# Kernel optimization log

Measured on AMD Instinct MI355X. Metric: run time of the kernel, lower is better.

## Reference

```python
import jax, jax.numpy as jnp
import numpy as np

B, S = 256, 32
XSIZE, YSIZE = 64, 64
LABEL_SIZE = 24
DEFAULT_LABEL = 0


def setup_inputs() -> dict:
    key = jax.random.key(0)
    ks = jax.random.split(key, 12)
    inp = {
        'pred_left': jax.random.normal(ks[0], (B, S, XSIZE), jnp.float32),
        'pred_top': jax.random.normal(ks[1], (B, S, YSIZE), jnp.float32),
        'pred_width': jax.random.normal(ks[2], (B, S, XSIZE), jnp.float32),
        'pred_height': jax.random.normal(ks[3], (B, S, YSIZE), jnp.float32),
        'pred_label': jax.random.normal(ks[4], (B, S, LABEL_SIZE), jnp.float32),
        'true_left': jax.random.randint(ks[5], (B, S), 0, XSIZE, jnp.int32),
        'true_top': jax.random.randint(ks[6], (B, S), 0, YSIZE, jnp.int32),
        'true_width': jax.random.randint(ks[7], (B, S), 0, 32, jnp.int32),
        'true_height': jax.random.randint(ks[8], (B, S), 0, 32, jnp.int32),
        'true_label': jax.random.randint(ks[9], (B, S), 0, LABEL_SIZE, jnp.int32),
        'true_length': jax.random.randint(ks[10], (B,), 0, S + 1, jnp.int32),
        'pred_length': jax.random.randint(ks[11], (B,), 0, S + 1, jnp.int32),
    }
    return inp


def _make_gridmaps(left, top, width, height, label, mask):
    right = jnp.minimum(XSIZE - 1, left + width)    # [B,S]
    bottom = jnp.minimum(YSIZE - 1, top + height)   # [B,S]
    # original skips boxes with top>=bottom or left>=right
    valid = mask & (top < bottom) & (left < right)
    ys = jnp.arange(YSIZE, dtype=jnp.int32)
    xs = jnp.arange(XSIZE, dtype=jnp.int32)
    cov_y = (top[:, :, None] <= ys) & (ys <= bottom[:, :, None])   # [B,S,Y]
    cov_x = (left[:, :, None] <= xs) & (xs <= right[:, :, None])   # [B,S,X]
    cover = valid[:, :, None, None] & cov_y[:, :, :, None] & cov_x[:, :, None, :]  # [B,S,Y,X]
    j = jnp.arange(S, dtype=jnp.int32)
    last = jnp.max(jnp.where(cover, j[None, :, None, None], -1), axis=1)  # [B,Y,X]
    gathered = jnp.take_along_axis(
        label, jnp.clip(last, 0, S - 1).reshape(label.shape[0], -1), axis=1
    ).reshape(last.shape)
    return jnp.where(last >= 0, gathered, DEFAULT_LABEL)


def _compute_acc_miou(map_true, map_pred):
    b = map_true.shape[0]
    bidx = jnp.arange(b, dtype=jnp.int32)[:, None]
    pred = map_pred.reshape(b, -1)
    true = map_true.reshape(b, -1)
    confusion = jnp.zeros((b, LABEL_SIZE, LABEL_SIZE), jnp.int32).at[bidx, pred, true].add(1)
    confusion = confusion.astype(jnp.float32)
    inter = jnp.diagonal(confusion, axis1=1, axis2=2)
    union = confusion.sum(axis=1) + confusion.sum(axis=2) - inter
    acc = inter.sum(axis=1) / confusion.sum(axis=(1, 2))
    weight = (union > 0).astype(jnp.float32)
    iou = inter / (union + 1e-9)
    miou = (weight * iou).sum(axis=1) / weight.sum(axis=1)
    return acc, miou


def reference(pred_left, pred_top, pred_width, pred_height, pred_label,
              true_left, true_top, true_width, true_height, true_label,
              true_length, pred_length):
    seq = jnp.arange(S, dtype=jnp.int32)
    mask_true = seq[None, :] < true_length[:, None]
    mask_pred = seq[None, :] < pred_length[:, None]
    map_true = _make_gridmaps(true_left, true_top, true_width, true_height,
                              true_label, mask_true)
    # from_logits: argmax over last dim (stop_gradient in original)
    pl = jnp.argmax(jax.lax.stop_gradient(pred_left), axis=-1).astype(jnp.int32)
    pt = jnp.argmax(jax.lax.stop_gradient(pred_top), axis=-1).astype(jnp.int32)
    pw = jnp.argmax(jax.lax.stop_gradient(pred_width), axis=-1).astype(jnp.int32)
    ph = jnp.argmax(jax.lax.stop_gradient(pred_height), axis=-1).astype(jnp.int32)
    plab = jnp.argmax(jax.lax.stop_gradient(pred_label), axis=-1).astype(jnp.int32)
    map_pred = _make_gridmaps(pl, pt, pw, ph, plab, mask_pred)
    acc, miou = _compute_acc_miou(map_true, map_pred)
    return acc, miou
```

## Files before the change

kernel.cpp:

```cpp
#include <hip/hip_runtime.h>

#define NB 256
#define S  32
#define NL 24

__global__ __launch_bounds__(256) void layout_metric_kernel(
    const float* __restrict__ pred_left,
    const float* __restrict__ pred_top,
    const float* __restrict__ pred_width,
    const float* __restrict__ pred_height,
    const float* __restrict__ pred_label,
    const int* __restrict__ true_left,
    const int* __restrict__ true_top,
    const int* __restrict__ true_width,
    const int* __restrict__ true_height,
    const int* __restrict__ true_label,
    const int* __restrict__ true_length,
    const int* __restrict__ pred_length,
    float* __restrict__ out)
{
    const int b   = blockIdx.x;
    const int tid = threadIdx.x;

    __shared__ int s_arg[5][S];
    __shared__ unsigned long long s_xmask[2][S];
    __shared__ unsigned int s_meta[2][S];
    __shared__ unsigned long long s_M[2][64][NL];
    __shared__ int s_cnt[3][NL];

    if (tid < 5 * S) {
        const int type = tid >> 5;
        const int j    = tid & 31;
        float best = -3.402823466e38f;
        int   bi   = 0;
        if (type < 4) {
            const float* base = (type == 0) ? pred_left
                              : (type == 1) ? pred_top
                              : (type == 2) ? pred_width
                                            : pred_height;
            const float4* r4 = (const float4*)(base + ((size_t)b * S + j) * 64);
            #pragma unroll
            for (int k = 0; k < 16; ++k) {
                float4 v = r4[k];
                if (v.x > best) { best = v.x; bi = 4 * k + 0; }
                if (v.y > best) { best = v.y; bi = 4 * k + 1; }
                if (v.z > best) { best = v.z; bi = 4 * k + 2; }
                if (v.w > best) { best = v.w; bi = 4 * k + 3; }
            }
        } else {
            const float4* r4 = (const float4*)(pred_label + ((size_t)b * S + j) * NL);
            #pragma unroll
            for (int k = 0; k < 6; ++k) {
                float4 v = r4[k];
                if (v.x > best) { best = v.x; bi = 4 * k + 0; }
                if (v.y > best) { best = v.y; bi = 4 * k + 1; }
                if (v.z > best) { best = v.z; bi = 4 * k + 2; }
                if (v.w > best) { best = v.w; bi = 4 * k + 3; }
            }
        }
        s_arg[type][j] = bi;
    }

    {
        unsigned long long* mflat = &s_M[0][0][0];
        #pragma unroll
        for (int k = 0; k < 12; ++k) mflat[tid + k * 256] = 0ull;
        if (tid < 3 * NL) (&s_cnt[0][0])[tid] = 0;
    }
    __syncthreads();

    if (tid < 2 * S) {
        const int m = tid >> 5;
        const int j = tid & 31;
        int l, t, w, h, lab, len;
        if (m == 0) {
            l   = true_left  [b * S + j];
            t   = true_top   [b * S + j];
            w   = true_width [b * S + j];
            h   = true_height[b * S + j];
            lab = true_label [b * S + j];
            len = true_length[b];
        } else {
            l   = s_arg[0][j];
            t   = s_arg[1][j];
            w   = s_arg[2][j];
            h   = s_arg[3][j];
            lab = s_arg[4][j];
            len = pred_length[b];
        }
        const int r  = min(63, l + w);
        const int bo = min(63, t + h);
        const bool val = (j < len) && (t < bo) && (l < r);
        unsigned long long xm = 0ull;
        if (val) xm = (~0ull << l) & (~0ull >> (63 - r));
        s_xmask[m][j] = xm;
        s_meta[m][j]  = (val ? 0x80000000u : 0u) |
                        ((unsigned)t << 12) | ((unsigned)bo << 6) | (unsigned)lab;
    }
    __syncthreads();

    if (tid < 128) {
        const int m = tid >> 6;
        const int y = tid & 63;
        unsigned long long rem = ~0ull;
        #pragma unroll
        for (int j = S - 1; j >= 0; --j) {
            const unsigned int md = s_meta[m][j];
            if (md & 0x80000000u) {
                const int top = (md >> 12) & 63;
                const int bot = (md >> 6)  & 63;
                if (top <= y && y <= bot) {
                    const unsigned long long cov = s_xmask[m][j] & rem;
                    if (cov) {
                        rem &= ~cov;
                        s_M[m][y][md & 31] |= cov;
                    }
                }
            }
        }
        if (rem) s_M[m][y][0] |= rem;
    }
    __syncthreads();

    if (tid < 8 * NL) {
        const int L  = tid >> 3;
        const int rg = tid & 7;
        int ct = 0, cp = 0, ci = 0;
        #pragma unroll
        for (int i = 0; i < 8; ++i) {
            const int y = rg * 8 + i;
            const unsigned long long tm = s_M[0][y][L];
            const unsigned long long pm = s_M[1][y][L];
            ct += __popcll(tm);
            cp += __popcll(pm);
            ci += __popcll(tm & pm);
        }
        atomicAdd(&s_cnt[0][L], ct);
        atomicAdd(&s_cnt[1][L], cp);
        atomicAdd(&s_cnt[2][L], ci);
    }
    __syncthreads();

    if (tid == 0) {
        int   it = 0;
        float ws = 0.f, wi = 0.f;
        #pragma unroll
        for (int L = 0; L < NL; ++L) {
            const int ct = s_cnt[0][L];
            const int cp = s_cnt[1][L];
            const int ci = s_cnt[2][L];
            const int un = ct + cp - ci;
            it += ci;
            if (un > 0) {
                ws += 1.f;
                wi += (float)ci / ((float)un + 1e-9f);
            }
        }
        out[b]      = (float)it / 4096.0f;
        out[NB + b] = wi / ws;
    }
}

extern "C" void kernel_launch(void* const* d_in, const int* in_sizes, int n_in,
                              void* d_out, int out_size, void* d_ws, size_t ws_size,
                              hipStream_t stream) {
    const float* pred_left   = (const float*)d_in[0];
    const float* pred_top    = (const float*)d_in[1];
    const float* pred_width  = (const float*)d_in[2];
    const float* pred_height = (const float*)d_in[3];
    const float* pred_label  = (const float*)d_in[4];
    const int*   true_left   = (const int*)d_in[5];
    const int*   true_top    = (const int*)d_in[6];
    const int*   true_width  = (const int*)d_in[7];
    const int*   true_height = (const int*)d_in[8];
    const int*   true_label  = (const int*)d_in[9];
    const int*   true_length = (const int*)d_in[10];
    const int*   pred_length = (const int*)d_in[11];
    float* out = (float*)d_out;

    layout_metric_kernel<<<NB, 256, 0, stream>>>(
        pred_left, pred_top, pred_width, pred_height, pred_label,
        true_left, true_top, true_width, true_height, true_label,
        true_length, pred_length, out);
}
```

Baseline: 15.48 us.

## Split argmax rows across thread pairs, overlap true-box setup, and shuffle-reduce the final metric

Doubles the block to 512 threads. Each 64-wide argmax row is now split between two threads that merge their results with a lane shuffle. The true-box mask setup and the counter zeroing run in other warps during the argmax phase, so one sync stage now handles only the predicted boxes. The final per-label sum moves from a single thread to a wavefront shuffle reduction, and the histogram thread mapping changes to reduce atomic contention on the same label. Larger blocks may lower occupancy, and the extra shuffles add some overhead.

```diff
diff --git a/kernel.cpp b/kernel.cpp
--- a/kernel.cpp
+++ b/kernel.cpp
@@ -4,7 +4,7 @@
 #define S  32
 #define NL 24
 
-__global__ __launch_bounds__(256) void layout_metric_kernel(
+__global__ __launch_bounds__(512) void layout_metric_kernel(
     const float* __restrict__ pred_left,
     const float* __restrict__ pred_top,
     const float* __restrict__ pred_width,
@@ -28,73 +28,88 @@
     __shared__ unsigned long long s_M[2][64][NL];
     __shared__ int s_cnt[3][NL];
 
-    if (tid < 5 * S) {
-        const int type = tid >> 5;
-        const int j    = tid & 31;
+    if (tid < 256) {
+        const int type = tid >> 6;
+        const int j    = (tid >> 1) & 31;
+        const int half = tid & 1;
+        const float* base = (type == 0) ? pred_left
+                          : (type == 1) ? pred_top
+                          : (type == 2) ? pred_width
+                                        : pred_height;
+        const float4* r4 = (const float4*)(base + ((size_t)b * S + j) * 64) + half * 8;
+        float best = -3.402823466e38f;
+        int   bi   = half * 32;
+        #pragma unroll
+        for (int k = 0; k < 8; ++k) {
+            float4 v = r4[k];
+            const int o = half * 32 + 4 * k;
+            if (v.x > best) { best = v.x; bi = o + 0; }
+            if (v.y > best) { best = v.y; bi = o + 1; }
+            if (v.z > best) { best = v.z; bi = o + 2; }
+            if (v.w > best) { best = v.w; bi = o + 3; }
+        }
+        const float ob = __shfl_xor(best, 1);
+        const int   oi = __shfl_xor(bi, 1);
+        if (half == 0) {
+            if (ob > best) { bi = oi; }
+            s_arg[type][j] = bi;
+        }
+    } else if (tid < 288) {
+        const int j = tid - 256;
+        const float4* r4 = (const float4*)(pred_label + ((size_t)b * S + j) * NL);
         float best = -3.402823466e38f;
         int   bi   = 0;
-        if (type < 4) {
-            const float* base = (type == 0) ? pred_left
-                              : (type == 1) ? pred_top
-                              : (type == 2) ? pred_width
-                                            : pred_height;
-            const float4* r4 = (const float4*)(base + ((size_t)b * S + j) * 64);
-            #pragma unroll
-            for (int k = 0; k < 16; ++k) {
-                float4 v = r4[k];
-                if (v.x > best) { best = v.x; bi = 4 * k + 0; }
-                if (v.y > best) { best = v.y; bi = 4 * k + 1; }
-                if (v.z > best) { best = v.z; bi = 4 * k + 2; }
-                if (v.w > best) { best = v.w; bi = 4 * k + 3; }
-            }
-        } else {
-            const float4* r4 = (const float4*)(pred_label + ((size_t)b * S + j) * NL);
-            #pragma unroll
-            for (int k = 0; k < 6; ++k) {
-                float4 v = r4[k];
-                if (v.x > best) { best = v.x; bi = 4 * k + 0; }
-                if (v.y > best) { best = v.y; bi = 4 * k + 1; }
-                if (v.z > best) { best = v.z; bi = 4 * k + 2; }
-                if (v.w > best) { best = v.w; bi = 4 * k + 3; }
-            }
-        }
-        s_arg[type][j] = bi;
-    }
-
-    {
-        unsigned long long* mflat = &s_M[0][0][0];
-        #pragma unroll
-        for (int k = 0; k < 12; ++k) mflat[tid + k * 256] = 0ull;
-        if (tid < 3 * NL) (&s_cnt[0][0])[tid] = 0;
-    }
-    __syncthreads();
-
-    if (tid < 2 * S) {
-        const int m = tid >> 5;
-        const int j = tid & 31;
-        int l, t, w, h, lab, len;
-        if (m == 0) {
-            l   = true_left  [b * S + j];
-            t   = true_top   [b * S + j];
-            w   = true_width [b * S + j];
-            h   = true_height[b * S + j];
-            lab = true_label [b * S + j];
-            len = true_length[b];
-        } else {
-            l   = s_arg[0][j];
-            t   = s_arg[1][j];
-            w   = s_arg[2][j];
-            h   = s_arg[3][j];
-            lab = s_arg[4][j];
-            len = pred_length[b];
-        }
+        #pragma unroll
+        for (int k = 0; k < 6; ++k) {
+            float4 v = r4[k];
+            if (v.x > best) { best = v.x; bi = 4 * k + 0; }
+            if (v.y > best) { best = v.y; bi = 4 * k + 1; }
+            if (v.z > best) { best = v.z; bi = 4 * k + 2; }
+            if (v.w > best) { best = v.w; bi = 4 * k + 3; }
+        }
+        s_arg[4][j] = bi;
+    } else if (tid >= 320 && tid < 352) {
+        const int j   = tid - 320;
+        const int l   = true_left  [b * S + j];
+        const int t   = true_top   [b * S + j];
+        const int w   = true_width [b * S + j];
+        const int h   = true_height[b * S + j];
+        const int lab = true_label [b * S + j];
+        const int len = true_length[b];
         const int r  = min(63, l + w);
         const int bo = min(63, t + h);
         const bool val = (j < len) && (t < bo) && (l < r);
         unsigned long long xm = 0ull;
         if (val) xm = (~0ull << l) & (~0ull >> (63 - r));
-        s_xmask[m][j] = xm;
-        s_meta[m][j]  = (val ? 0x80000000u : 0u) |
+        s_xmask[0][j] = xm;
+        s_meta[0][j]  = (val ? 0x80000000u : 0u) |
+                        ((unsigned)t << 12) | ((unsigned)bo << 6) | (unsigned)lab;
+    } else if (tid >= 352 && tid < 352 + 3 * NL) {
+        (&s_cnt[0][0])[tid - 352] = 0;
+    }
+
+    {
+        unsigned long long* mflat = &s_M[0][0][0];
+        #pragma unroll
+        for (int k = 0; k < 6; ++k) mflat[tid + k * 512] = 0ull;
+    }
+    __syncthreads();
+
+    if (tid < S) {
+        const int j   = tid;
+        const int l   = s_arg[0][j];
+        const int t   = s_arg[1][j];
+        const int w   = s_arg[2][j];
+        const int h   = s_arg[3][j];
+        const int lab = s_arg[4][j];
+        const int len = pred_length[b];
+        const int r  = min(63, l + w);
+        const int bo = min(63, t + h);
+        const bool val = (j < len) && (t < bo) && (l < r);
+        unsigned long long xm = 0ull;
+        if (val) xm = (~0ull << l) & (~0ull >> (63 - r));
+        s_xmask[1][j] = xm;
+        s_meta[1][j]  = (val ? 0x80000000u : 0u) |
                         ((unsigned)t << 12) | ((unsigned)bo << 6) | (unsigned)lab;
     }
     __syncthreads();
@@ -123,8 +138,8 @@
     __syncthreads();
 
     if (tid < 8 * NL) {
-        const int L  = tid >> 3;
-        const int rg = tid & 7;
+        const int L  = tid % NL;
+        const int rg = tid / NL;
         int ct = 0, cp = 0, ci = 0;
         #pragma unroll
         for (int i = 0; i < 8; ++i) {
@@ -141,23 +156,29 @@
     }
     __syncthreads();
 
-    if (tid == 0) {
-        int   it = 0;
-        float ws = 0.f, wi = 0.f;
-        #pragma unroll
-        for (int L = 0; L < NL; ++L) {
-            const int ct = s_cnt[0][L];
-            const int cp = s_cnt[1][L];
-            const int ci = s_cnt[2][L];
+    if (tid < 64) {
+        float it_p = 0.f, ws_p = 0.f, wi_p = 0.f;
+        if (tid < NL) {
+            const int ct = s_cnt[0][tid];
+            const int cp = s_cnt[1][tid];
+            const int ci = s_cnt[2][tid];
             const int un = ct + cp - ci;
-            it += ci;
+            it_p = (float)ci;
             if (un > 0) {
-                ws += 1.f;
-                wi += (float)ci / ((float)un + 1e-9f);
+                ws_p = 1.f;
+                wi_p = (float)ci / ((float)un + 1e-9f);
             }
         }
-        out[b]      = (float)it / 4096.0f;
-        out[NB + b] = wi / ws;
+        #pragma unroll
+        for (int m = 32; m >= 1; m >>= 1) {
+            it_p += __shfl_xor(it_p, m);
+            ws_p += __shfl_xor(ws_p, m);
+            wi_p += __shfl_xor(wi_p, m);
+        }
+        if (tid == 0) {
+            out[b]      = it_p / 4096.0f;
+            out[NB + b] = wi_p / ws_p;
+        }
     }
 }
 
@@ -178,7 +199,7 @@
     const int*   pred_length = (const int*)d_in[11];
     float* out = (float*)d_out;
 
-    layout_metric_kernel<<<NB, 256, 0, stream>>>(
+    layout_metric_kernel<<<NB, 512, 0, stream>>>(
         pred_left, pred_top, pred_width, pred_height, pred_label,
         true_left, true_top, true_width, true_height, true_label,
         true_length, pred_length, out);
```

Result: faster. 13.07 us (-15.6%).
